# Performance work log

Hardware: AMD Instinct MI355X
Metric: run time of the kernel (lower is better)

## Reference

```python
import jax, jax.numpy as jnp
import numpy as np

MAX_TOP_K = 3
NUM_EXPERTS = 64
B, S, D = 4, 4096, 4096
H = D // 2


def setup_inputs() -> dict:
    key = jax.random.key(0)
    k0, k1, k2, k3 = jax.random.split(key, 4)
    x = jax.random.normal(k0, (B, S, D), dtype=jnp.float32)
    W = jax.random.normal(k1, (D, NUM_EXPERTS), dtype=jnp.float32) * 0.1
    # top_k_predictor: Linear(D, D//2) -> ReLU -> Linear(D//2, 1) -> Sigmoid
    W1 = jax.random.normal(k2, (D, H), dtype=jnp.float32) * (1.0 / np.sqrt(D))
    b1 = jnp.zeros((H,), dtype=jnp.float32)
    W2 = jax.random.normal(k3, (H, 1), dtype=jnp.float32) * (1.0 / np.sqrt(H))
    b2 = jnp.zeros((1,), dtype=jnp.float32)
    return {"x": x, "W": W, "W1": W1, "b1": b1, "W2": W2, "b2": b2}


def reference(x, W, W1, b1, W2, b2):
    b, s, d = x.shape
    x_flat = x.reshape(-1, d)                                  # [N, D]
    n = x_flat.shape[0]

    # small predictor MLP -> per-token dynamic k
    h = jax.nn.relu(x_flat @ W1 + b1)                          # [N, H]
    top_k_scores = jax.nn.sigmoid(h @ W2 + b2)[:, 0]           # [N]
    dynamic_top_k = jnp.clip(
        jnp.round(top_k_scores * MAX_TOP_K) + 1.0, 1.0, float(MAX_TOP_K)
    ).astype(jnp.int32)                                        # [N]

    # gating matmul + softmax + top-k
    gate_probs = jax.nn.softmax(x_flat @ W, axis=-1)           # [N, E]
    top_k_probs, top_k_indices = jax.lax.top_k(gate_probs, MAX_TOP_K)  # [N, K]

    # per-token dynamic-k mask and renormalize
    k_mask = jnp.arange(MAX_TOP_K)[None, :] < dynamic_top_k[:, None]   # [N, K]
    top_k_probs = top_k_probs * k_mask.astype(top_k_probs.dtype)
    top_k_weights = top_k_probs / (top_k_probs.sum(-1, keepdims=True) + 1e-8)

    # routing mask: 1 where expert is in top-k AND its (masked) weight > 0
    rows = jnp.arange(n)[:, None]                              # [N, 1]
    routing_mask = jnp.zeros((n, NUM_EXPERTS), top_k_weights.dtype).at[
        rows, top_k_indices
    ].set((top_k_weights > 0).astype(top_k_weights.dtype))     # [N, E]

    return (
        top_k_weights,
        top_k_indices,
        routing_mask.reshape(b, s, NUM_EXPERTS),
        dynamic_top_k,
    )
```

## Files before the change

### kernel.cpp

```cpp
#include <hip/hip_runtime.h>
#include <hip/hip_bf16.h>
#include <math.h>

#define DD   4096
#define HH   2048
#define NE   64
#define BK   32
#define NT   16
#define GM   32

typedef __attribute__((ext_vector_type(8))) short bf16x8;
typedef __attribute__((ext_vector_type(4))) float f32x4;

__device__ __forceinline__ void async16(void* lds, const void* g) {
    __builtin_amdgcn_global_load_lds(
        (const __attribute__((address_space(1))) unsigned int*)g,
        (__attribute__((address_space(3))) unsigned int*)lds, 16, 0, 0);
}

__device__ __forceinline__ void split2(float a, float b, unsigned& hi, unsigned& lo) {
    __hip_bfloat162 h = __float22bfloat162_rn(make_float2(a, b));
    float2 hf = __bfloat1622float2(h);
    __hip_bfloat162 l = __float22bfloat162_rn(make_float2(a - hf.x, b - hf.y));
    __builtin_memcpy(&hi, &h, 4);
    __builtin_memcpy(&lo, &l, 4);
}

__global__ __launch_bounds__(256) void split_x(
    const float4* __restrict__ x, uint4* __restrict__ xh, uint4* __restrict__ xl,
    long n8)
{
    long i = (long)blockIdx.x * 256 + threadIdx.x;
    if (i >= n8) return;
    float4 a = x[2 * i], b = x[2 * i + 1];
    unsigned h0, l0, h1, l1, h2, l2, h3, l3;
    split2(a.x, a.y, h0, l0); split2(a.z, a.w, h1, l1);
    split2(b.x, b.y, h2, l2); split2(b.z, b.w, h3, l3);
    xh[i] = make_uint4(h0, h1, h2, h3);
    xl[i] = make_uint4(l0, l1, l2, l3);
}

__global__ __launch_bounds__(256) void split_w1t(
    const float* __restrict__ W1,
    unsigned short* __restrict__ th, unsigned short* __restrict__ tl)
{
    __shared__ float ts[32][33];
    const int n0 = blockIdx.x * 32, k0 = blockIdx.y * 32;
    const int t = threadIdx.x;
    {
        int r = t >> 3, c4 = (t & 7) * 4;
        float4 v = *(const float4*)&W1[(size_t)(k0 + r) * HH + n0 + c4];
        ts[r][c4] = v.x; ts[r][c4 + 1] = v.y; ts[r][c4 + 2] = v.z; ts[r][c4 + 3] = v.w;
    }
    __syncthreads();
    int n = t >> 3, kk = (t & 7) * 4;
    float f0 = ts[kk][n], f1 = ts[kk + 1][n], f2 = ts[kk + 2][n], f3 = ts[kk + 3][n];
    unsigned h0, l0, h1, l1;
    split2(f0, f1, h0, l0); split2(f2, f3, h1, l1);
    *(uint2*)&th[(size_t)(n0 + n) * DD + k0 + kk] = make_uint2(h0, h1);
    *(uint2*)&tl[(size_t)(n0 + n) * DD + k0 + kk] = make_uint2(l0, l1);
}

template<bool PRE_A>
__global__ __launch_bounds__(256, 3) void pred_mfma(
    const float* __restrict__ x,
    const unsigned short* __restrict__ xh, const unsigned short* __restrict__ xl,
    const unsigned short* __restrict__ w1th, const unsigned short* __restrict__ w1tl,
    const float* __restrict__ b1, const float* __restrict__ W2,
    double* __restrict__ pl)
{
    __shared__ __align__(16) char lds[32768];
    char* Ah = lds;
    char* Al = lds + 8192;
    char* Bh = lds + 16384;
    char* Bl = lds + 24576;

    const int t = threadIdx.x, wv = t >> 6, ln = t & 63;
    const int lin = blockIdx.x;
    const int sub = lin >> 3;
    const int ntile = (lin & 7) * 2 + (sub & 1);
    const int mtile = sub >> 1;
    const int m0 = mtile * 128, n0 = ntile * 128;
    const int frow = ln & 15;
    const int fkb  = (ln >> 4) * 8;

    f32x4 acc[4][4];
#pragma unroll
    for (int i = 0; i < 4; ++i)
#pragma unroll
        for (int j = 0; j < 4; ++j) acc[i][j] = (f32x4){0.f, 0.f, 0.f, 0.f};

    const unsigned short* rsrc = nullptr; char* rdst = nullptr; size_t rbase = 0;
    if (PRE_A) {
        if (wv == 0)      { rsrc = xh;   rbase = (size_t)(m0 + frow) * DD; rdst = Ah; }
        else if (wv == 1) { rsrc = xl;   rbase = (size_t)(m0 + frow) * DD; rdst = Al; }
        else if (wv == 2) { rsrc = w1th; rbase = (size_t)(n0 + frow) * DD; rdst = Bh; }
        else              { rsrc = w1tl; rbase = (size_t)(n0 + frow) * DD; rdst = Bl; }
    }
    const unsigned short* gBh = w1th + (size_t)(n0 + frow) * DD + fkb;
    const unsigned short* gBl = w1tl + (size_t)(n0 + frow) * DD + fkb;

    const int mb = (wv & 1) * 4, nb = (wv >> 1) * 4;

    if (PRE_A) {
        {
            const unsigned short* g = rsrc + rbase + fkb;
#pragma unroll
            for (int fb = 0; fb < 8; ++fb)
                async16(rdst + fb * 1024, g + (size_t)fb * 16 * DD);
        }
        for (int kc = 0; kc < DD; kc += BK) {
            __syncthreads();

            bf16x8 afh[4], afl[4], bfh[4], bfl[4];
#pragma unroll
            for (int i = 0; i < 4; ++i) {
                afh[i] = *(const bf16x8*)(Ah + (mb + i) * 1024 + ln * 16);
                afl[i] = *(const bf16x8*)(Al + (mb + i) * 1024 + ln * 16);
                bfh[i] = *(const bf16x8*)(Bh + (nb + i) * 1024 + ln * 16);
                bfl[i] = *(const bf16x8*)(Bl + (nb + i) * 1024 + ln * 16);
            }
            __syncthreads();

            if (kc + BK < DD) {
                const unsigned short* g = rsrc + rbase + (kc + BK) + fkb;
#pragma unroll
                for (int fb = 0; fb < 8; ++fb)
                    async16(rdst + fb * 1024, g + (size_t)fb * 16 * DD);
            }

#pragma unroll
            for (int i = 0; i < 4; ++i)
#pragma unroll
                for (int j = 0; j < 4; ++j) {
                    acc[i][j] = __builtin_amdgcn_mfma_f32_16x16x32_bf16(afh[i], bfh[j], acc[i][j], 0, 0, 0);
                    acc[i][j] = __builtin_amdgcn_mfma_f32_16x16x32_bf16(afh[i], bfl[j], acc[i][j], 0, 0, 0);
                    acc[i][j] = __builtin_amdgcn_mfma_f32_16x16x32_bf16(afl[i], bfh[j], acc[i][j], 0, 0, 0);
                }
        }
    } else {
        for (int kc = 0; kc < DD; kc += BK) {
#pragma unroll
            for (int q = 0; q < 2; ++q) {
                int fb = wv * 2 + q;
                async16(Bh + fb * 1024, gBh + (size_t)fb * 16 * DD + kc);
                async16(Bl + fb * 1024, gBl + (size_t)fb * 16 * DD + kc);
            }
#pragma unroll
            for (int s2 = 0; s2 < 2; ++s2) {
                int s = t + s2 * 256;
                int fb = s >> 6, sl = s & 63;
                int row = fb * 16 + (sl & 15), kb = (sl >> 4) * 8;
                const float* g = x + (size_t)(m0 + row) * DD + kc + kb;
                float4 a = *(const float4*)g, b = *(const float4*)(g + 4);
                unsigned h0, l0, h1, l1, h2, l2, h3, l3;
                split2(a.x, a.y, h0, l0); split2(a.z, a.w, h1, l1);
                split2(b.x, b.y, h2, l2); split2(b.z, b.w, h3, l3);
                *(uint4*)(Ah + s * 16) = make_uint4(h0, h1, h2, h3);
                *(uint4*)(Al + s * 16) = make_uint4(l0, l1, l2, l3);
            }
            __syncthreads();

            bf16x8 afh[4], afl[4], bfh[4], bfl[4];
#pragma unroll
            for (int i = 0; i < 4; ++i) {
                afh[i] = *(const bf16x8*)(Ah + (mb + i) * 1024 + ln * 16);
                afl[i] = *(const bf16x8*)(Al + (mb + i) * 1024 + ln * 16);
                bfh[i] = *(const bf16x8*)(Bh + (nb + i) * 1024 + ln * 16);
                bfl[i] = *(const bf16x8*)(Bl + (nb + i) * 1024 + ln * 16);
            }
#pragma unroll
            for (int i = 0; i < 4; ++i)
#pragma unroll
                for (int j = 0; j < 4; ++j) {
                    acc[i][j] = __builtin_amdgcn_mfma_f32_16x16x32_bf16(afh[i], bfh[j], acc[i][j], 0, 0, 0);
                    acc[i][j] = __builtin_amdgcn_mfma_f32_16x16x32_bf16(afh[i], bfl[j], acc[i][j], 0, 0, 0);
                    acc[i][j] = __builtin_amdgcn_mfma_f32_16x16x32_bf16(afl[i], bfh[j], acc[i][j], 0, 0, 0);
                }
            __syncthreads();
        }
    }

    __syncthreads();
    double* redd = (double*)lds;
    const int mh = wv & 1, nh = wv >> 1;
    float b1v[4], w2v[4];
#pragma unroll
    for (int j = 0; j < 4; ++j) {
        int col = n0 + nh * 64 + j * 16 + frow;
        b1v[j] = b1[col];
        w2v[j] = W2[col];
    }
#pragma unroll
    for (int i = 0; i < 4; ++i)
#pragma unroll
        for (int r = 0; r < 4; ++r) {
            double s = 0.0;
#pragma unroll
            for (int j = 0; j < 4; ++j) {
                float h = acc[i][j][r] + b1v[j];
                h = fmaxf(h, 0.f);
                s += (double)h * (double)w2v[j];
            }
#pragma unroll
            for (int o = 1; o < 16; o <<= 1) s += __shfl_xor(s, o, 64);
            if (frow == 0)
                redd[nh * 128 + mh * 64 + i * 16 + (ln >> 4) * 4 + r] = s;
        }
    __syncthreads();
    if (t < 128)
        pl[(size_t)(m0 + t) * NT + ntile] = redd[t] + redd[128 + t];
}

__global__ __launch_bounds__(256) void pred_gemm(
    const float* __restrict__ x, const float* __restrict__ W1,
    const float* __restrict__ b1, const float* __restrict__ W2,
    double* __restrict__ pl)
{
    __shared__ float As[BK][128];
    __shared__ float Bs[BK][128];
    __shared__ double red[128][NT + 1];

    const int ht = blockIdx.x;
    const int tm = blockIdx.y;
    const int t  = threadIdx.x;
    const int tx = t & 15, ty = t >> 4;
    const int h0 = ht * 128;
    const int m0 = tm * 128;

    float acc[8][8];
#pragma unroll
    for (int i = 0; i < 8; ++i)
#pragma unroll
        for (int j = 0; j < 8; ++j) acc[i][j] = 0.f;

    const int arow = t >> 1, acol = (t & 1) << 4;
    const int brow = t >> 3, bcol = (t & 7) << 4;
    const float* xrow = x  + (size_t)(m0 + arow) * DD + acol;
    const float* wrow = W1 + (size_t)brow * HH + h0 + bcol;

    for (int k0 = 0; k0 < DD; k0 += BK) {
        float4 a4[4], b4[4];
        const float4* ap = (const float4*)(xrow + k0);
#pragma unroll
        for (int i = 0; i < 4; ++i) a4[i] = ap[i];
        const float4* bp = (const float4*)(wrow + (size_t)k0 * HH);
#pragma unroll
        for (int i = 0; i < 4; ++i) b4[i] = bp[i];
        __syncthreads();
#pragma unroll
        for (int i = 0; i < 4; ++i) {
            As[acol + i * 4 + 0][arow] = a4[i].x;
            As[acol + i * 4 + 1][arow] = a4[i].y;
            As[acol + i * 4 + 2][arow] = a4[i].z;
            As[acol + i * 4 + 3][arow] = a4[i].w;
        }
#pragma unroll
        for (int i = 0; i < 4; ++i)
            *(float4*)&Bs[brow][bcol + i * 4] = b4[i];
        __syncthreads();
#pragma unroll 8
        for (int kk = 0; kk < BK; ++kk) {
            float4 a0  = *(const float4*)&As[kk][ty * 8];
            float4 a1  = *(const float4*)&As[kk][ty * 8 + 4];
            float4 bb0 = *(const float4*)&Bs[kk][tx * 8];
            float4 bb1 = *(const float4*)&Bs[kk][tx * 8 + 4];
            float av[8] = {a0.x, a0.y, a0.z, a0.w, a1.x, a1.y, a1.z, a1.w};
            float bv[8] = {bb0.x, bb0.y, bb0.z, bb0.w, bb1.x, bb1.y, bb1.z, bb1.w};
#pragma unroll
            for (int i = 0; i < 8; ++i)
#pragma unroll
                for (int j = 0; j < 8; ++j)
                    acc[i][j] = fmaf(av[i], bv[j], acc[i][j]);
        }
    }
    __syncthreads();
#pragma unroll
    for (int r = 0; r < 8; ++r) {
        double s = 0.0;
#pragma unroll
        for (int c = 0; c < 8; ++c) {
            int h = h0 + tx * 8 + c;
            float v = acc[r][c] + b1[h];
            v = v > 0.f ? v : 0.f;
            s += (double)v * (double)W2[h];
        }
        red[ty * 8 + r][tx] = s;
    }
    __syncthreads();
    if (t < 128) {
        double s = 0.0;
#pragma unroll
        for (int j = 0; j < NT; ++j) s += red[t][j];
        pl[(size_t)(m0 + t) * NT + ht] = s;
    }
}

__global__ __launch_bounds__(256) void gate_fused(
    const float* __restrict__ x, const float* __restrict__ W,
    const double* __restrict__ pl, const float* __restrict__ b2,
    float* __restrict__ out, int Ntok)
{
    __shared__ __align__(16) char smem[GM * (NE + 1) * sizeof(double)];
    float (*As)[GM] = (float(*)[GM])smem;
    float (*Bs)[NE] = (float(*)[NE])(smem + BK * GM * 4);
    double (*Dm)[NE + 1] = (double(*)[NE + 1])smem;

    const int tm = blockIdx.x;
    const int t  = threadIdx.x;
    const int tx = t & 15, ty = t >> 4;
    const int m0 = tm * GM;

    double acc[2][4];
#pragma unroll
    for (int i = 0; i < 2; ++i)
#pragma unroll
        for (int j = 0; j < 4; ++j) acc[i][j] = 0.0;

    const int arow = t >> 3, acol = (t & 7) * 4;
    const int brow = t >> 3, bcol = (t & 7) * 8;
    const float* xrow = x + (size_t)(m0 + arow) * DD + acol;
    const float* wrow = W + (size_t)brow * NE + bcol;

    float4 a4  = *(const float4*)xrow;
    float4 b40 = *(const float4*)wrow;
    float4 b41 = *(const float4*)(wrow + 4);

    for (int k0 = 0; k0 < DD; k0 += BK) {
        __syncthreads();
        As[acol + 0][arow] = a4.x;
        As[acol + 1][arow] = a4.y;
        As[acol + 2][arow] = a4.z;
        As[acol + 3][arow] = a4.w;
        *(float4*)&Bs[brow][bcol]     = b40;
        *(float4*)&Bs[brow][bcol + 4] = b41;
        __syncthreads();

        if (k0 + BK < DD) {
            a4  = *(const float4*)(xrow + k0 + BK);
            b40 = *(const float4*)(wrow + (size_t)(k0 + BK) * NE);
            b41 = *(const float4*)(wrow + (size_t)(k0 + BK) * NE + 4);
        }

#pragma unroll 8
        for (int kk = 0; kk < BK; ++kk) {
            double a0 = (double)As[kk][ty * 2];
            double a1 = (double)As[kk][ty * 2 + 1];
            float4 b = *(const float4*)&Bs[kk][tx * 4];
            double bv[4] = {(double)b.x, (double)b.y, (double)b.z, (double)b.w};
#pragma unroll
            for (int j = 0; j < 4; ++j) {
                acc[0][j] = fma(a0, bv[j], acc[0][j]);
                acc[1][j] = fma(a1, bv[j], acc[1][j]);
            }
        }
    }

    __syncthreads();
#pragma unroll
    for (int r = 0; r < 2; ++r)
#pragma unroll
        for (int c = 0; c < 4; ++c)
            Dm[ty * 2 + r][tx * 4 + c] = acc[r][c];
    __syncthreads();

    const int wave = t >> 6;
    const int lane = t & 63;
    const double b2v = (double)b2[0];

    for (int i = 0; i < 8; ++i) {
        const int tl = wave * 8 + i;
        const int token = m0 + tl;
        double g = Dm[tl][lane];

        double mx = g;
#pragma unroll
        for (int o = 32; o > 0; o >>= 1) mx = fmax(mx, __shfl_xor(mx, o, 64));
        double e = exp(g - mx);
        double s = e;
#pragma unroll
        for (int o = 32; o > 0; o >>= 1) s += __shfl_xor(s, o, 64);
        double p = e / s;

        double pv = p; int pi = lane;
        double vt[3]; int it[3];
#pragma unroll
        for (int j = 0; j < 3; ++j) {
            double v = pv; int idx = pi;
#pragma unroll
            for (int o = 32; o > 0; o >>= 1) {
                double ov = __shfl_xor(v, o, 64);
                int    oi = __shfl_xor(idx, o, 64);
                if (ov > v || (ov == v && oi < idx)) { v = ov; idx = oi; }
            }
            vt[j] = v; it[j] = idx;
            if (lane == idx) pv = -1.0;
        }

        double plv = (lane < NT) ? pl[(size_t)token * NT + lane] : 0.0;
#pragma unroll
        for (int o = 32; o > 0; o >>= 1) plv += __shfl_xor(plv, o, 64);
        double logit = plv + b2v;
        double score = 1.0 / (1.0 + exp(-logit));
        int k = (int)rint(score * 3.0) + 1;
        k = k < 1 ? 1 : (k > 3 ? 3 : k);

        double wmask[3]; double wsum = 0.0;
#pragma unroll
        for (int j = 0; j < 3; ++j) { wmask[j] = (j < k) ? vt[j] : 0.0; wsum += wmask[j]; }
        double denom = wsum + 1e-8;
        float wn[3];
#pragma unroll
        for (int j = 0; j < 3; ++j) wn[j] = (float)(wmask[j] / denom);

        float mval = 0.f;
#pragma unroll
        for (int j = 0; j < 3; ++j)
            if (it[j] == lane && wn[j] > 0.f) mval = 1.f;

        out[(size_t)6 * Ntok + (size_t)token * NE + lane] = mval;
        if (lane < 3) {
            out[(size_t)token * 3 + lane] = wn[lane];
            out[(size_t)3 * Ntok + (size_t)token * 3 + lane] = (float)it[lane];
        }
        if (lane == 0) out[(size_t)70 * Ntok + token] = (float)k;
    }
}

extern "C" void kernel_launch(void* const* d_in, const int* in_sizes, int n_in,
                              void* d_out, int out_size, void* d_ws, size_t ws_size,
                              hipStream_t stream)
{
    const float* x  = (const float*)d_in[0];
    const float* W  = (const float*)d_in[1];
    const float* W1 = (const float*)d_in[2];
    const float* b1 = (const float*)d_in[3];
    const float* W2 = (const float*)d_in[4];
    const float* b2 = (const float*)d_in[5];
    float* out = (float*)d_out;

    const int Ntok = in_sizes[0] / DD;

    double* pl = (double*)d_ws;
    const size_t pl_b   = (size_t)Ntok * NT * sizeof(double);
    const size_t o_w1h  = (pl_b + 255) & ~(size_t)255;
    const size_t w1_b   = (size_t)DD * HH * 2;
    const size_t o_w1l  = o_w1h + w1_b;
    const size_t o_xh   = o_w1l + w1_b;
    const size_t x_b    = (size_t)Ntok * DD * 2;
    const size_t o_xl   = o_xh + x_b;
    const size_t need_w1   = o_xh;
    const size_t need_full = o_xl + x_b;

    const bool ok128 = (Ntok % 128) == 0;

    if (ok128 && ws_size >= need_w1) {
        unsigned short* w1th = (unsigned short*)((char*)d_ws + o_w1h);
        unsigned short* w1tl = (unsigned short*)((char*)d_ws + o_w1l);
        split_w1t<<<dim3(HH / 32, DD / 32), 256, 0, stream>>>(W1, w1th, w1tl);
        if (ws_size >= need_full) {
            unsigned short* xh = (unsigned short*)((char*)d_ws + o_xh);
            unsigned short* xl = (unsigned short*)((char*)d_ws + o_xl);
            long n8 = (long)Ntok * DD / 8;
            split_x<<<(int)((n8 + 255) / 256), 256, 0, stream>>>(
                (const float4*)x, (uint4*)xh, (uint4*)xl, n8);
            pred_mfma<true><<<16 * (Ntok / 128), 256, 0, stream>>>(
                x, xh, xl, w1th, w1tl, b1, W2, pl);
        } else {
            pred_mfma<false><<<16 * (Ntok / 128), 256, 0, stream>>>(
                x, nullptr, nullptr, w1th, w1tl, b1, W2, pl);
        }
    } else {
        pred_gemm<<<dim3(NT, Ntok / 128), 256, 0, stream>>>(x, W1, b1, W2, pl);
    }

    gate_fused<<<Ntok / GM, 256, 0, stream>>>(x, W, pl, b2, out, Ntok);
}
```

Before: 1.753 ms.

## Double-buffer LDS in predictor MFMA GEMM and enlarge gate kernel per-thread tile

Measured after the change: 2.005 ms. 14.4% more time.

```diff
diff --git a/kernel.cpp b/kernel.cpp
--- a/kernel.cpp
+++ b/kernel.cpp
@@ -62,18 +62,14 @@
 }
 
 template<bool PRE_A>
-__global__ __launch_bounds__(256, 3) void pred_mfma(
+__global__ __launch_bounds__(256, 2) void pred_mfma(
     const float* __restrict__ x,
     const unsigned short* __restrict__ xh, const unsigned short* __restrict__ xl,
     const unsigned short* __restrict__ w1th, const unsigned short* __restrict__ w1tl,
     const float* __restrict__ b1, const float* __restrict__ W2,
     double* __restrict__ pl)
 {
-    __shared__ __align__(16) char lds[32768];
-    char* Ah = lds;
-    char* Al = lds + 8192;
-    char* Bh = lds + 16384;
-    char* Bl = lds + 24576;
+    __shared__ __align__(16) char lds[65536];
 
     const int t = threadIdx.x, wv = t >> 6, ln = t & 63;
     const int lin = blockIdx.x;
@@ -90,43 +86,42 @@
 #pragma unroll
         for (int j = 0; j < 4; ++j) acc[i][j] = (f32x4){0.f, 0.f, 0.f, 0.f};
 
-    const unsigned short* rsrc = nullptr; char* rdst = nullptr; size_t rbase = 0;
+    const int mb = (wv & 1) * 4, nb = (wv >> 1) * 4;
+
     if (PRE_A) {
-        if (wv == 0)      { rsrc = xh;   rbase = (size_t)(m0 + frow) * DD; rdst = Ah; }
-        else if (wv == 1) { rsrc = xl;   rbase = (size_t)(m0 + frow) * DD; rdst = Al; }
-        else if (wv == 2) { rsrc = w1th; rbase = (size_t)(n0 + frow) * DD; rdst = Bh; }
-        else              { rsrc = w1tl; rbase = (size_t)(n0 + frow) * DD; rdst = Bl; }
-    }
-    const unsigned short* gBh = w1th + (size_t)(n0 + frow) * DD + fkb;
-    const unsigned short* gBl = w1tl + (size_t)(n0 + frow) * DD + fkb;
-
-    const int mb = (wv & 1) * 4, nb = (wv >> 1) * 4;
-
-    if (PRE_A) {
+        const unsigned short* rsrc; size_t rbase; int roff;
+        if (wv == 0)      { rsrc = xh;   rbase = (size_t)(m0 + frow) * DD; roff = 0; }
+        else if (wv == 1) { rsrc = xl;   rbase = (size_t)(m0 + frow) * DD; roff = 8192; }
+        else if (wv == 2) { rsrc = w1th; rbase = (size_t)(n0 + frow) * DD; roff = 16384; }
+        else              { rsrc = w1tl; rbase = (size_t)(n0 + frow) * DD; roff = 24576; }
+
         {
             const unsigned short* g = rsrc + rbase + fkb;
 #pragma unroll
             for (int fb = 0; fb < 8; ++fb)
-                async16(rdst + fb * 1024, g + (size_t)fb * 16 * DD);
-        }
+                async16(lds + roff + fb * 1024, g + (size_t)fb * 16 * DD);
+        }
+        __syncthreads();
+
+        int cur = 0;
         for (int kc = 0; kc < DD; kc += BK) {
-            __syncthreads();
-
-            bf16x8 afh[4], afl[4], bfh[4], bfl[4];
-#pragma unroll
-            for (int i = 0; i < 4; ++i) {
-                afh[i] = *(const bf16x8*)(Ah + (mb + i) * 1024 + ln * 16);
-                afl[i] = *(const bf16x8*)(Al + (mb + i) * 1024 + ln * 16);
-                bfh[i] = *(const bf16x8*)(Bh + (nb + i) * 1024 + ln * 16);
-                bfl[i] = *(const bf16x8*)(Bl + (nb + i) * 1024 + ln * 16);
-            }
-            __syncthreads();
+            char* R = lds + (cur << 15);
+            char* S = lds + ((cur ^ 1) << 15);
 
             if (kc + BK < DD) {
                 const unsigned short* g = rsrc + rbase + (kc + BK) + fkb;
 #pragma unroll
                 for (int fb = 0; fb < 8; ++fb)
-                    async16(rdst + fb * 1024, g + (size_t)fb * 16 * DD);
+                    async16(S + roff + fb * 1024, g + (size_t)fb * 16 * DD);
+            }
+
+            bf16x8 afh[4], afl[4], bfh[4], bfl[4];
+#pragma unroll
+            for (int i = 0; i < 4; ++i) {
+                afh[i] = *(const bf16x8*)(R         + (mb + i) * 1024 + ln * 16);
+                afl[i] = *(const bf16x8*)(R + 8192  + (mb + i) * 1024 + ln * 16);
+                bfh[i] = *(const bf16x8*)(R + 16384 + (nb + i) * 1024 + ln * 16);
+                bfl[i] = *(const bf16x8*)(R + 24576 + (nb + i) * 1024 + ln * 16);
             }
 
 #pragma unroll
@@ -137,8 +132,18 @@
                     acc[i][j] = __builtin_amdgcn_mfma_f32_16x16x32_bf16(afh[i], bfl[j], acc[i][j], 0, 0, 0);
                     acc[i][j] = __builtin_amdgcn_mfma_f32_16x16x32_bf16(afl[i], bfh[j], acc[i][j], 0, 0, 0);
                 }
+
+            __syncthreads();
+            cur ^= 1;
         }
     } else {
+        char* Ah = lds;
+        char* Al = lds + 8192;
+        char* Bh = lds + 16384;
+        char* Bl = lds + 24576;
+        const unsigned short* gBh = w1th + (size_t)(n0 + frow) * DD + fkb;
+        const unsigned short* gBl = w1tl + (size_t)(n0 + frow) * DD + fkb;
+
         for (int kc = 0; kc < DD; kc += BK) {
 #pragma unroll
             for (int q = 0; q < 2; ++q) {
@@ -296,7 +301,7 @@
     }
 }
 
-__global__ __launch_bounds__(256) void gate_fused(
+__global__ __launch_bounds__(128) void gate_fused(
     const float* __restrict__ x, const float* __restrict__ W,
     const double* __restrict__ pl, const float* __restrict__ b2,
     float* __restrict__ out, int Ntok)
@@ -311,65 +316,74 @@
     const int tx = t & 15, ty = t >> 4;
     const int m0 = tm * GM;
 
-    double acc[2][4];
-#pragma unroll
-    for (int i = 0; i < 2; ++i)
+    double acc[4][4];
+#pragma unroll
+    for (int i = 0; i < 4; ++i)
 #pragma unroll
         for (int j = 0; j < 4; ++j) acc[i][j] = 0.0;
 
-    const int arow = t >> 3, acol = (t & 7) * 4;
-    const int brow = t >> 3, bcol = (t & 7) * 8;
+    const int arow = t >> 2, acol = (t & 3) * 8;
+    const int brow = t >> 2, bcol = (t & 3) * 16;
     const float* xrow = x + (size_t)(m0 + arow) * DD + acol;
     const float* wrow = W + (size_t)brow * NE + bcol;
 
-    float4 a4  = *(const float4*)xrow;
-    float4 b40 = *(const float4*)wrow;
-    float4 b41 = *(const float4*)(wrow + 4);
+    float4 a40 = *(const float4*)xrow;
+    float4 a41 = *(const float4*)(xrow + 4);
+    float4 b4[4];
+#pragma unroll
+    for (int i = 0; i < 4; ++i) b4[i] = *(const float4*)(wrow + i * 4);
 
     for (int k0 = 0; k0 < DD; k0 += BK) {
         __syncthreads();
-        As[acol + 0][arow] = a4.x;
-        As[acol + 1][arow] = a4.y;
-        As[acol + 2][arow] = a4.z;
-        As[acol + 3][arow] = a4.w;
-        *(float4*)&Bs[brow][bcol]     = b40;
-        *(float4*)&Bs[brow][bcol + 4] = b41;
+        As[acol + 0][arow] = a40.x;
+        As[acol + 1][arow] = a40.y;
+        As[acol + 2][arow] = a40.z;
+        As[acol + 3][arow] = a40.w;
+        As[acol + 4][arow] = a41.x;
+        As[acol + 5][arow] = a41.y;
+        As[acol + 6][arow] = a41.z;
+        As[acol + 7][arow] = a41.w;
+#pragma unroll
+        for (int i = 0; i < 4; ++i)
+            *(float4*)&Bs[brow][bcol + i * 4] = b4[i];
         __syncthreads();
 
         if (k0 + BK < DD) {
-            a4  = *(const float4*)(xrow + k0 + BK);
-            b40 = *(const float4*)(wrow + (size_t)(k0 + BK) * NE);
-            b41 = *(const float4*)(wrow + (size_t)(k0 + BK) * NE + 4);
+            a40 = *(const float4*)(xrow + k0 + BK);
+            a41 = *(const float4*)(xrow + k0 + BK + 4);
+#pragma unroll
+            for (int i = 0; i < 4; ++i)
+                b4[i] = *(const float4*)(wrow + (size_t)(k0 + BK) * NE + i * 4);
         }
 
 #pragma unroll 8
         for (int kk = 0; kk < BK; ++kk) {
-            double a0 = (double)As[kk][ty * 2];
-            double a1 = (double)As[kk][ty * 2 + 1];
+            float4 a = *(const float4*)&As[kk][ty * 4];
             float4 b = *(const float4*)&Bs[kk][tx * 4];
+            double av[4] = {(double)a.x, (double)a.y, (double)a.z, (double)a.w};
             double bv[4] = {(double)b.x, (double)b.y, (double)b.z, (double)b.w};
 #pragma unroll
-            for (int j = 0; j < 4; ++j) {
-                acc[0][j] = fma(a0, bv[j], acc[0][j]);
-                acc[1][j] = fma(a1, bv[j], acc[1][j]);
-            }
-        }
-    }
-
-    __syncthreads();
-#pragma unroll
-    for (int r = 0; r < 2; ++r)
+            for (int r = 0; r < 4; ++r)
+#pragma unroll
+                for (int c = 0; c < 4; ++c)
+                    acc[r][c] = fma(av[r], bv[c], acc[r][c]);
+        }
+    }
+
+    __syncthreads();
+#pragma unroll
+    for (int r = 0; r < 4; ++r)
 #pragma unroll
         for (int c = 0; c < 4; ++c)
-            Dm[ty * 2 + r][tx * 4 + c] = acc[r][c];
+            Dm[ty * 4 + r][tx * 4 + c] = acc[r][c];
     __syncthreads();
 
     const int wave = t >> 6;
     const int lane = t & 63;
     const double b2v = (double)b2[0];
 
-    for (int i = 0; i < 8; ++i) {
-        const int tl = wave * 8 + i;
+    for (int i = 0; i < 16; ++i) {
+        const int tl = wave * 16 + i;
         const int token = m0 + tl;
         double g = Dm[tl][lane];
 
@@ -474,5 +488,5 @@
         pred_gemm<<<dim3(NT, Ntok / 128), 256, 0, stream>>>(x, W1, b1, W2, pl);
     }
 
-    gate_fused<<<Ntok / GM, 256, 0, stream>>>(x, W, pl, b2, out, Ntok);
-}
+    gate_fused<<<Ntok / GM, 128, 0, stream>>>(x, W, pl, b2, out, Ntok);
+}
```

## Pre-swizzle x into MFMA fragment layout and load A directly to registers

Applied to the files above, without the earlier changes.

Result: faster. 1.703 ms (-2.8%).

```diff
diff --git a/kernel.cpp b/kernel.cpp
--- a/kernel.cpp
+++ b/kernel.cpp
@@ -8,6 +8,8 @@
 #define BK   32
 #define NT   16
 #define GM   32
+#define GMP  (GM + 2)
+#define NEP  (NE + 2)
 
 typedef __attribute__((ext_vector_type(8))) short bf16x8;
 typedef __attribute__((ext_vector_type(4))) float f32x4;
@@ -26,18 +28,27 @@
     __builtin_memcpy(&lo, &l, 4);
 }
 
-__global__ __launch_bounds__(256) void split_x(
-    const float4* __restrict__ x, uint4* __restrict__ xh, uint4* __restrict__ xl,
-    long n8)
+__global__ __launch_bounds__(256) void split_xf(
+    const float* __restrict__ x, uint4* __restrict__ xfh, uint4* __restrict__ xfl)
 {
-    long i = (long)blockIdx.x * 256 + threadIdx.x;
-    if (i >= n8) return;
-    float4 a = x[2 * i], b = x[2 * i + 1];
-    unsigned h0, l0, h1, l1, h2, l2, h3, l3;
-    split2(a.x, a.y, h0, l0); split2(a.z, a.w, h1, l1);
-    split2(b.x, b.y, h2, l2); split2(b.z, b.w, h3, l3);
-    xh[i] = make_uint4(h0, h1, h2, h3);
-    xl[i] = make_uint4(l0, l1, l2, l3);
+    const int t = threadIdx.x;
+    const int mt = blockIdx.x >> 7;
+    const int ks = blockIdx.x & 127;
+#pragma unroll
+    for (int s2 = 0; s2 < 2; ++s2) {
+        int s = t + s2 * 256;
+        int fb = s >> 6, ln = s & 63;
+        int row = mt * 128 + fb * 16 + (ln & 15);
+        int k   = ks * 32 + (ln >> 4) * 8;
+        const float* g = x + (size_t)row * DD + k;
+        float4 a = *(const float4*)g, b = *(const float4*)(g + 4);
+        unsigned h0, l0, h1, l1, h2, l2, h3, l3;
+        split2(a.x, a.y, h0, l0); split2(a.z, a.w, h1, l1);
+        split2(b.x, b.y, h2, l2); split2(b.z, b.w, h3, l3);
+        size_t idx = ((size_t)blockIdx.x * 8 + fb) * 64 + ln;
+        xfh[idx] = make_uint4(h0, h1, h2, h3);
+        xfl[idx] = make_uint4(l0, l1, l2, l3);
+    }
 }
 
 __global__ __launch_bounds__(256) void split_w1t(
@@ -70,10 +81,6 @@
     double* __restrict__ pl)
 {
     __shared__ __align__(16) char lds[32768];
-    char* Ah = lds;
-    char* Al = lds + 8192;
-    char* Bh = lds + 16384;
-    char* Bl = lds + 24576;
 
     const int t = threadIdx.x, wv = t >> 6, ln = t & 63;
     const int lin = blockIdx.x;
@@ -90,55 +97,82 @@
 #pragma unroll
         for (int j = 0; j < 4; ++j) acc[i][j] = (f32x4){0.f, 0.f, 0.f, 0.f};
 
-    const unsigned short* rsrc = nullptr; char* rdst = nullptr; size_t rbase = 0;
+    const int mb = (wv & 1) * 4, nb = (wv >> 1) * 4;
+
     if (PRE_A) {
-        if (wv == 0)      { rsrc = xh;   rbase = (size_t)(m0 + frow) * DD; rdst = Ah; }
-        else if (wv == 1) { rsrc = xl;   rbase = (size_t)(m0 + frow) * DD; rdst = Al; }
-        else if (wv == 2) { rsrc = w1th; rbase = (size_t)(n0 + frow) * DD; rdst = Bh; }
-        else              { rsrc = w1tl; rbase = (size_t)(n0 + frow) * DD; rdst = Bl; }
-    }
-    const unsigned short* gBh = w1th + (size_t)(n0 + frow) * DD + fkb;
-    const unsigned short* gBl = w1tl + (size_t)(n0 + frow) * DD + fkb;
-
-    const int mb = (wv & 1) * 4, nb = (wv >> 1) * 4;
-
-    if (PRE_A) {
-        {
-            const unsigned short* g = rsrc + rbase + fkb;
-#pragma unroll
-            for (int fb = 0; fb < 8; ++fb)
-                async16(rdst + fb * 1024, g + (size_t)fb * 16 * DD);
-        }
-        for (int kc = 0; kc < DD; kc += BK) {
+        char* Bh = lds;
+        char* Bl = lds + 8192;
+
+        const unsigned short* bsrc = (wv & 2) ? w1tl : w1th;
+        const int fb0 = (wv & 1) * 4;
+        char* bdst = ((wv & 2) ? Bl : Bh) + fb0 * 1024;
+        const unsigned short* bg =
+            bsrc + (size_t)(n0 + fb0 * 16 + frow) * DD + fkb;
+
+        const uint4* gh = (const uint4*)xh + ((size_t)mtile * 1024 + mb) * 64 + ln;
+        const uint4* gl = (const uint4*)xl + ((size_t)mtile * 1024 + mb) * 64 + ln;
+
+        bf16x8 ah[4], al[4];
+
+#pragma unroll
+        for (int q = 0; q < 4; ++q)
+            async16(bdst + q * 1024, bg + (size_t)q * 16 * DD);
+#pragma unroll
+        for (int i = 0; i < 4; ++i) {
+            ah[i] = *(const bf16x8*)(gh + i * 64);
+            al[i] = *(const bf16x8*)(gl + i * 64);
+        }
+
+        for (int ks = 0; ks < 128; ++ks) {
             __syncthreads();
 
-            bf16x8 afh[4], afl[4], bfh[4], bfl[4];
-#pragma unroll
-            for (int i = 0; i < 4; ++i) {
-                afh[i] = *(const bf16x8*)(Ah + (mb + i) * 1024 + ln * 16);
-                afl[i] = *(const bf16x8*)(Al + (mb + i) * 1024 + ln * 16);
-                bfh[i] = *(const bf16x8*)(Bh + (nb + i) * 1024 + ln * 16);
-                bfl[i] = *(const bf16x8*)(Bl + (nb + i) * 1024 + ln * 16);
+            bf16x8 bfh[4], bfl[4];
+#pragma unroll
+            for (int j = 0; j < 4; ++j) {
+                bfh[j] = *(const bf16x8*)(Bh + (nb + j) * 1024 + ln * 16);
+                bfl[j] = *(const bf16x8*)(Bl + (nb + j) * 1024 + ln * 16);
             }
             __syncthreads();
 
-            if (kc + BK < DD) {
-                const unsigned short* g = rsrc + rbase + (kc + BK) + fkb;
-#pragma unroll
-                for (int fb = 0; fb < 8; ++fb)
-                    async16(rdst + fb * 1024, g + (size_t)fb * 16 * DD);
+            const bool more = (ks + 1 < 128);
+            if (more) {
+#pragma unroll
+                for (int q = 0; q < 4; ++q)
+                    async16(bdst + q * 1024,
+                            bg + (size_t)q * 16 * DD + (ks + 1) * BK);
             }
 
 #pragma unroll
             for (int i = 0; i < 4; ++i)
 #pragma unroll
                 for (int j = 0; j < 4; ++j) {
-                    acc[i][j] = __builtin_amdgcn_mfma_f32_16x16x32_bf16(afh[i], bfh[j], acc[i][j], 0, 0, 0);
-                    acc[i][j] = __builtin_amdgcn_mfma_f32_16x16x32_bf16(afh[i], bfl[j], acc[i][j], 0, 0, 0);
-                    acc[i][j] = __builtin_amdgcn_mfma_f32_16x16x32_bf16(afl[i], bfh[j], acc[i][j], 0, 0, 0);
+                    acc[i][j] = __builtin_amdgcn_mfma_f32_16x16x32_bf16(ah[i], bfh[j], acc[i][j], 0, 0, 0);
+                    acc[i][j] = __builtin_amdgcn_mfma_f32_16x16x32_bf16(ah[i], bfl[j], acc[i][j], 0, 0, 0);
                 }
+            if (more) {
+#pragma unroll
+                for (int i = 0; i < 4; ++i)
+                    ah[i] = *(const bf16x8*)(gh + (size_t)(ks + 1) * 512 + i * 64);
+            }
+#pragma unroll
+            for (int i = 0; i < 4; ++i)
+#pragma unroll
+                for (int j = 0; j < 4; ++j)
+                    acc[i][j] = __builtin_amdgcn_mfma_f32_16x16x32_bf16(al[i], bfh[j], acc[i][j], 0, 0, 0);
+            if (more) {
+#pragma unroll
+                for (int i = 0; i < 4; ++i)
+                    al[i] = *(const bf16x8*)(gl + (size_t)(ks + 1) * 512 + i * 64);
+            }
         }
     } else {
+        char* Ah = lds;
+        char* Al = lds + 8192;
+        char* Bh = lds + 16384;
+        char* Bl = lds + 24576;
+        const unsigned short* gBh = w1th + (size_t)(n0 + frow) * DD + fkb;
+        const unsigned short* gBl = w1tl + (size_t)(n0 + frow) * DD + fkb;
+
         for (int kc = 0; kc < DD; kc += BK) {
 #pragma unroll
             for (int q = 0; q < 2; ++q) {
@@ -301,9 +335,9 @@
     const double* __restrict__ pl, const float* __restrict__ b2,
     float* __restrict__ out, int Ntok)
 {
-    __shared__ __align__(16) char smem[GM * (NE + 1) * sizeof(double)];
-    float (*As)[GM] = (float(*)[GM])smem;
-    float (*Bs)[NE] = (float(*)[NE])(smem + BK * GM * 4);
+    __shared__ __align__(16) char smem[(BK * GMP + BK * NEP) * 8];
+    double (*Asd)[GMP] = (double(*)[GMP])smem;
+    double (*Bsd)[NEP] = (double(*)[NEP])(smem + BK * GMP * 8);
     double (*Dm)[NE + 1] = (double(*)[NE + 1])smem;
 
     const int tm = blockIdx.x;
@@ -328,12 +362,18 @@
 
     for (int k0 = 0; k0 < DD; k0 += BK) {
         __syncthreads();
-        As[acol + 0][arow] = a4.x;
-        As[acol + 1][arow] = a4.y;
-        As[acol + 2][arow] = a4.z;
-        As[acol + 3][arow] = a4.w;
-        *(float4*)&Bs[brow][bcol]     = b40;
-        *(float4*)&Bs[brow][bcol + 4] = b41;
+        Asd[acol + 0][arow] = (double)a4.x;
+        Asd[acol + 1][arow] = (double)a4.y;
+        Asd[acol + 2][arow] = (double)a4.z;
+        Asd[acol + 3][arow] = (double)a4.w;
+        Bsd[brow][bcol + 0] = (double)b40.x;
+        Bsd[brow][bcol + 1] = (double)b40.y;
+        Bsd[brow][bcol + 2] = (double)b40.z;
+        Bsd[brow][bcol + 3] = (double)b40.w;
+        Bsd[brow][bcol + 4] = (double)b41.x;
+        Bsd[brow][bcol + 5] = (double)b41.y;
+        Bsd[brow][bcol + 6] = (double)b41.z;
+        Bsd[brow][bcol + 7] = (double)b41.w;
         __syncthreads();
 
         if (k0 + BK < DD) {
@@ -344,14 +384,14 @@
 
 #pragma unroll 8
         for (int kk = 0; kk < BK; ++kk) {
-            double a0 = (double)As[kk][ty * 2];
-            double a1 = (double)As[kk][ty * 2 + 1];
-            float4 b = *(const float4*)&Bs[kk][tx * 4];
-            double bv[4] = {(double)b.x, (double)b.y, (double)b.z, (double)b.w};
+            double2 av  = *(const double2*)&Asd[kk][ty * 2];
+            double2 bv0 = *(const double2*)&Bsd[kk][tx * 4];
+            double2 bv1 = *(const double2*)&Bsd[kk][tx * 4 + 2];
+            double bv[4] = {bv0.x, bv0.y, bv1.x, bv1.y};
 #pragma unroll
             for (int j = 0; j < 4; ++j) {
-                acc[0][j] = fma(a0, bv[j], acc[0][j]);
-                acc[1][j] = fma(a1, bv[j], acc[1][j]);
+                acc[0][j] = fma(av.x, bv[j], acc[0][j]);
+                acc[1][j] = fma(av.y, bv[j], acc[1][j]);
             }
         }
     }
@@ -459,13 +499,11 @@
         unsigned short* w1tl = (unsigned short*)((char*)d_ws + o_w1l);
         split_w1t<<<dim3(HH / 32, DD / 32), 256, 0, stream>>>(W1, w1th, w1tl);
         if (ws_size >= need_full) {
-            unsigned short* xh = (unsigned short*)((char*)d_ws + o_xh);
-            unsigned short* xl = (unsigned short*)((char*)d_ws + o_xl);
-            long n8 = (long)Ntok * DD / 8;
-            split_x<<<(int)((n8 + 255) / 256), 256, 0, stream>>>(
-                (const float4*)x, (uint4*)xh, (uint4*)xl, n8);
+            unsigned short* xfh = (unsigned short*)((char*)d_ws + o_xh);
+            unsigned short* xfl = (unsigned short*)((char*)d_ws + o_xl);
+            split_xf<<<Ntok, 256, 0, stream>>>(x, (uint4*)xfh, (uint4*)xfl);
             pred_mfma<true><<<16 * (Ntok / 128), 256, 0, stream>>>(
-                x, xh, xl, w1th, w1tl, b1, W2, pl);
+                x, xfh, xfl, w1th, w1tl, b1, W2, pl);
         } else {
             pred_mfma<false><<<16 * (Ntok / 128), 256, 0, stream>>>(
                 x, nullptr, nullptr, w1th, w1tl, b1, W2, pl);
```

## Pre-swizzle x into MFMA fragment layout and load A directly to registers

Applied to the files above, without the earlier changes.

Measured after the change: 1.895 ms. 1.08x slower.

```diff
diff --git a/kernel.cpp b/kernel.cpp
--- a/kernel.cpp
+++ b/kernel.cpp
@@ -26,18 +26,27 @@
     __builtin_memcpy(&lo, &l, 4);
 }
 
-__global__ __launch_bounds__(256) void split_x(
-    const float4* __restrict__ x, uint4* __restrict__ xh, uint4* __restrict__ xl,
-    long n8)
+__global__ __launch_bounds__(256) void split_xf(
+    const float* __restrict__ x, uint4* __restrict__ xfh, uint4* __restrict__ xfl)
 {
-    long i = (long)blockIdx.x * 256 + threadIdx.x;
-    if (i >= n8) return;
-    float4 a = x[2 * i], b = x[2 * i + 1];
-    unsigned h0, l0, h1, l1, h2, l2, h3, l3;
-    split2(a.x, a.y, h0, l0); split2(a.z, a.w, h1, l1);
-    split2(b.x, b.y, h2, l2); split2(b.z, b.w, h3, l3);
-    xh[i] = make_uint4(h0, h1, h2, h3);
-    xl[i] = make_uint4(l0, l1, l2, l3);
+    const int t = threadIdx.x;
+    const int mt = blockIdx.x >> 7;
+    const int ks = blockIdx.x & 127;
+#pragma unroll
+    for (int s2 = 0; s2 < 2; ++s2) {
+        int s = t + s2 * 256;
+        int fb = s >> 6, ln = s & 63;
+        int row = mt * 128 + fb * 16 + (ln & 15);
+        int k   = ks * 32 + (ln >> 4) * 8;
+        const float* g = x + (size_t)row * DD + k;
+        float4 a = *(const float4*)g, b = *(const float4*)(g + 4);
+        unsigned h0, l0, h1, l1, h2, l2, h3, l3;
+        split2(a.x, a.y, h0, l0); split2(a.z, a.w, h1, l1);
+        split2(b.x, b.y, h2, l2); split2(b.z, b.w, h3, l3);
+        size_t idx = ((size_t)blockIdx.x * 8 + fb) * 64 + ln;
+        xfh[idx] = make_uint4(h0, h1, h2, h3);
+        xfl[idx] = make_uint4(l0, l1, l2, l3);
+    }
 }
 
 __global__ __launch_bounds__(256) void split_w1t(
@@ -70,10 +79,6 @@
     double* __restrict__ pl)
 {
     __shared__ __align__(16) char lds[32768];
-    char* Ah = lds;
-    char* Al = lds + 8192;
-    char* Bh = lds + 16384;
-    char* Bl = lds + 24576;
 
     const int t = threadIdx.x, wv = t >> 6, ln = t & 63;
     const int lin = blockIdx.x;
@@ -90,55 +95,84 @@
 #pragma unroll
         for (int j = 0; j < 4; ++j) acc[i][j] = (f32x4){0.f, 0.f, 0.f, 0.f};
 
-    const unsigned short* rsrc = nullptr; char* rdst = nullptr; size_t rbase = 0;
+    const int mb = (wv & 1) * 4, nb = (wv >> 1) * 4;
+
     if (PRE_A) {
-        if (wv == 0)      { rsrc = xh;   rbase = (size_t)(m0 + frow) * DD; rdst = Ah; }
-        else if (wv == 1) { rsrc = xl;   rbase = (size_t)(m0 + frow) * DD; rdst = Al; }
-        else if (wv == 2) { rsrc = w1th; rbase = (size_t)(n0 + frow) * DD; rdst = Bh; }
-        else              { rsrc = w1tl; rbase = (size_t)(n0 + frow) * DD; rdst = Bl; }
-    }
-    const unsigned short* gBh = w1th + (size_t)(n0 + frow) * DD + fkb;
-    const unsigned short* gBl = w1tl + (size_t)(n0 + frow) * DD + fkb;
-
-    const int mb = (wv & 1) * 4, nb = (wv >> 1) * 4;
-
-    if (PRE_A) {
-        {
-            const unsigned short* g = rsrc + rbase + fkb;
-#pragma unroll
-            for (int fb = 0; fb < 8; ++fb)
-                async16(rdst + fb * 1024, g + (size_t)fb * 16 * DD);
-        }
-        for (int kc = 0; kc < DD; kc += BK) {
-            __syncthreads();
-
-            bf16x8 afh[4], afl[4], bfh[4], bfl[4];
-#pragma unroll
-            for (int i = 0; i < 4; ++i) {
-                afh[i] = *(const bf16x8*)(Ah + (mb + i) * 1024 + ln * 16);
-                afl[i] = *(const bf16x8*)(Al + (mb + i) * 1024 + ln * 16);
-                bfh[i] = *(const bf16x8*)(Bh + (nb + i) * 1024 + ln * 16);
-                bfl[i] = *(const bf16x8*)(Bl + (nb + i) * 1024 + ln * 16);
-            }
-            __syncthreads();
-
-            if (kc + BK < DD) {
-                const unsigned short* g = rsrc + rbase + (kc + BK) + fkb;
-#pragma unroll
-                for (int fb = 0; fb < 8; ++fb)
-                    async16(rdst + fb * 1024, g + (size_t)fb * 16 * DD);
-            }
-
-#pragma unroll
-            for (int i = 0; i < 4; ++i)
-#pragma unroll
-                for (int j = 0; j < 4; ++j) {
-                    acc[i][j] = __builtin_amdgcn_mfma_f32_16x16x32_bf16(afh[i], bfh[j], acc[i][j], 0, 0, 0);
-                    acc[i][j] = __builtin_amdgcn_mfma_f32_16x16x32_bf16(afh[i], bfl[j], acc[i][j], 0, 0, 0);
-                    acc[i][j] = __builtin_amdgcn_mfma_f32_16x16x32_bf16(afl[i], bfh[j], acc[i][j], 0, 0, 0);
-                }
-        }
+        const unsigned short* bsrc = (wv & 2) ? w1tl : w1th;
+        const int roleoff = ((wv & 2) ? 8192 : 0) + (wv & 1) * 4096;
+        const unsigned short* bg =
+            bsrc + (size_t)(n0 + (wv & 1) * 64 + frow) * DD + fkb;
+
+        const uint4* gh = (const uint4*)xh + ((size_t)mtile * 1024 + mb) * 64 + ln;
+        const uint4* gl = (const uint4*)xl + ((size_t)mtile * 1024 + mb) * 64 + ln;
+
+        bf16x8 ah[4], alA[4], alB[4];
+
+#pragma unroll
+        for (int q = 0; q < 4; ++q)
+            async16(lds + roleoff + q * 1024, bg + (size_t)q * 16 * DD);
+#pragma unroll
+        for (int i = 0; i < 4; ++i) {
+            ah[i]  = *(const bf16x8*)(gh + i * 64);
+            alA[i] = *(const bf16x8*)(gl + i * 64);
+        }
+
+#define PRED_STEP(KS, RBOFF, SBOFF, alC, alN)                                  \
+        {                                                                      \
+            __syncthreads();  \
+            const bool more = (KS) + 1 < 128;                                  \
+            if (more) {                                                        \
+                              \
+                _Pragma("unroll")                                              \
+                for (int i = 0; i < 4; ++i)                                    \
+                    alN[i] = *(const bf16x8*)(gh_l + (size_t)((KS)+1) * 512 + i * 64); \
+                                     \
+                _Pragma("unroll")                                              \
+                for (int q = 0; q < 4; ++q)                                    \
+                    async16(lds + (SBOFF) + roleoff + q * 1024,                \
+                            bg + (size_t)q * 16 * DD + ((KS)+1) * BK);         \
+            }                                                                  \
+            bf16x8 bfh[4], bfl[4];                                             \
+            _Pragma("unroll")                                                  \
+            for (int j = 0; j < 4; ++j) {                                      \
+                bfh[j] = *(const bf16x8*)(lds + (RBOFF) + (nb + j) * 1024 + ln * 16);        \
+                bfl[j] = *(const bf16x8*)(lds + (RBOFF) + 8192 + (nb + j) * 1024 + ln * 16); \
+            }                                                                  \
+                                         \
+            _Pragma("unroll")                                                  \
+            for (int i = 0; i < 4; ++i)                                        \
+                _Pragma("unroll")                                              \
+                for (int j = 0; j < 4; ++j) {                                  \
+                    acc[i][j] = __builtin_amdgcn_mfma_f32_16x16x32_bf16(ah[i], bfh[j], acc[i][j], 0, 0, 0); \
+                    acc[i][j] = __builtin_amdgcn_mfma_f32_16x16x32_bf16(ah[i], bfl[j], acc[i][j], 0, 0, 0); \
+                }                                                              \
+            if (more) {                                                        \
+                _Pragma("unroll")                                              \
+                for (int i = 0; i < 4; ++i)                                    \
+                    ah[i] = *(const bf16x8*)(gh + (size_t)((KS)+1) * 512 + i * 64); \
+            }                                                                  \
+                                           \
+            _Pragma("unroll")                                                  \
+            for (int i = 0; i < 4; ++i)                                        \
+                _Pragma("unroll")                                              \
+                for (int j = 0; j < 4; ++j)                                    \
+                    acc[i][j] = __builtin_amdgcn_mfma_f32_16x16x32_bf16(alC[i], bfh[j], acc[i][j], 0, 0, 0); \
+        }
+
+        const uint4* gh_l = gl;
+        for (int ks = 0; ks < 128; ks += 2) {
+            PRED_STEP(ks,     0,     16384, alA, alB);
+            PRED_STEP(ks + 1, 16384, 0,     alB, alA);
+        }
+#undef PRED_STEP
     } else {
+        char* Ah = lds;
+        char* Al = lds + 8192;
+        char* Bh = lds + 16384;
+        char* Bl = lds + 24576;
+        const unsigned short* gBh = w1th + (size_t)(n0 + frow) * DD + fkb;
+        const unsigned short* gBl = w1tl + (size_t)(n0 + frow) * DD + fkb;
+
         for (int kc = 0; kc < DD; kc += BK) {
 #pragma unroll
             for (int q = 0; q < 2; ++q) {
@@ -459,13 +493,11 @@
         unsigned short* w1tl = (unsigned short*)((char*)d_ws + o_w1l);
         split_w1t<<<dim3(HH / 32, DD / 32), 256, 0, stream>>>(W1, w1th, w1tl);
         if (ws_size >= need_full) {
-            unsigned short* xh = (unsigned short*)((char*)d_ws + o_xh);
-            unsigned short* xl = (unsigned short*)((char*)d_ws + o_xl);
-            long n8 = (long)Ntok * DD / 8;
-            split_x<<<(int)((n8 + 255) / 256), 256, 0, stream>>>(
-                (const float4*)x, (uint4*)xh, (uint4*)xl, n8);
+            unsigned short* xfh = (unsigned short*)((char*)d_ws + o_xh);
+            unsigned short* xfl = (unsigned short*)((char*)d_ws + o_xl);
+            split_xf<<<Ntok, 256, 0, stream>>>(x, (uint4*)xfh, (uint4*)xfl);
             pred_mfma<true><<<16 * (Ntok / 128), 256, 0, stream>>>(
-                x, xh, xl, w1th, w1tl, b1, W2, pl);
+                x, xfh, xfl, w1th, w1tl, b1, W2, pl);
         } else {
             pred_mfma<false><<<16 * (Ntok / 128), 256, 0, stream>>>(
                 x, nullptr, nullptr, w1th, w1tl, b1, W2, pl);
```
